# Optimization experiments

Hardware: AMD Instinct MI355X
Metric: run time of the kernel (lower is better)

The kernel has to match this reference:

```python
import jax, jax.numpy as jnp
import numpy as np

NUM_FEATURES = 5
MUL_FACTOR = 2.0


def setup_inputs() -> dict:
    key = jax.random.key(0)
    x = jax.random.normal(key, (4096, 512), dtype=jnp.float32)
    # buffer from __init__: mul_factor ** (arange(F) - F // 2)
    bandwidth_multipliers = (MUL_FACTOR ** (jnp.arange(NUM_FEATURES) - NUM_FEATURES // 2)).astype(jnp.float32)
    return {"x": x, "bandwidth_multipliers": bandwidth_multipliers}


def _cdist(x):
    # pairwise Euclidean distance, p=2
    sq = jnp.sum(x * x, axis=1)
    d2 = sq[:, None] + sq[None, :] - 2.0 * (x @ x.T)
    return jnp.sqrt(jnp.maximum(d2, 0.0))


def reference(x, bandwidth_multipliers):
    d = _cdist(x)  # [N, N]
    n = d.shape[0]
    # heuristic bandwidth on detached distances (self.bandwidth is None)
    bw = jax.lax.stop_gradient(d).sum() / (n * (n - 1))
    bws = bw * bandwidth_multipliers  # [F]
    # exp over F bandwidths, summed: [F, N, N] -> [N, N]
    return jnp.exp(-d[None, :, :] / bws[:, None, None]).sum(axis=0)
```

## Files before the change

### kernel.cpp

```cpp
#include <hip/hip_runtime.h>
#include <cstdint>
#include <cstddef>

#define N_PTS 4096
#define KDIM  512
#define NFEAT 5

typedef __attribute__((ext_vector_type(8))) short bf16x8;
typedef __attribute__((ext_vector_type(4))) float f32x4;
typedef uint32_t u32;

__device__ inline unsigned short f2bf(float f) {
  union { float f; u32 u; } v; v.f = f;
  u32 r = (v.u + 0x7fffu + ((v.u >> 16) & 1u)) >> 16;
  return (unsigned short)r;
}

__device__ inline void bf2f2(u32 u, float& a, float& b) {
  union { u32 u; float f; } x, y;
  x.u = u << 16; y.u = u & 0xffff0000u;
  a = x.f; b = y.f;
}

__device__ inline void load_lds16(const void* g, void* l) {
  __builtin_amdgcn_global_load_lds(
      (const __attribute__((address_space(1))) void*)g,
      (__attribute__((address_space(3))) void*)l, 16, 0, 0);
}

__global__ __launch_bounds__(256) void prep_kernel(const float* __restrict__ X,
                                                   short* __restrict__ Xb,
                                                   float* __restrict__ sq) {
  const int row = blockIdx.x;
  const int t = threadIdx.x;
  const float2 v = ((const float2*)(X + (size_t)row * KDIM))[t];
  short2 b;
  b.x = (short)f2bf(v.x);
  b.y = (short)f2bf(v.y);
  ((short2*)(Xb + (size_t)row * KDIM))[t] = b;
  float s = v.x * v.x + v.y * v.y;
#pragma unroll
  for (int off = 32; off; off >>= 1) s += __shfl_down(s, off);
  __shared__ float ws[4];
  if ((t & 63) == 0) ws[t >> 6] = s;
  __syncthreads();
  if (t == 0) sq[row] = ws[0] + ws[1] + ws[2] + ws[3];
}

__global__ __launch_bounds__(256, 2) void dist_kernel(
    const short* __restrict__ Xb, const float* __restrict__ sq,
    unsigned short* __restrict__ Dw, float* __restrict__ gsum) {
  const int bm = blockIdx.y, bn = blockIdx.x;
  if (bm > bn) return;

  __shared__ short As[128 * 64];
  __shared__ short Bs[128 * 64];
  __shared__ float red[4];

  const int tid = threadIdx.x;
  const int lane = tid & 63;
  const int wid = tid >> 6;
  const int wave_m = wid >> 1, wave_n = wid & 1;
  const int lhi = lane >> 4, llo = lane & 15;

  f32x4 acc[4][4];
#pragma unroll
  for (int i = 0; i < 4; ++i)
#pragma unroll
    for (int j = 0; j < 4; ++j) acc[i][j] = (f32x4){0.f, 0.f, 0.f, 0.f};

  const int srow = tid >> 3;
  const int scol = (tid & 7) * 8;
  const size_t ga0 = (size_t)(bm * 128 + srow) * KDIM + scol;
  const size_t gb0 = (size_t)(bn * 128 + srow) * KDIM + scol;

  for (int kt = 0; kt < KDIM / 64; ++kt) {
    const int koff = kt * 64;
#pragma unroll
    for (int g = 0; g < 4; ++g) {
      load_lds16(Xb + ga0 + (size_t)g * 32 * KDIM + koff, (char*)As + g * 4096 + tid * 16);
      load_lds16(Xb + gb0 + (size_t)g * 32 * KDIM + koff, (char*)Bs + g * 4096 + tid * 16);
    }
    __syncthreads();

    bf16x8 a[2][4], b[2][4];
#pragma unroll
    for (int h = 0; h < 2; ++h)
#pragma unroll
      for (int i = 0; i < 4; ++i) {
        a[h][i] = *(const bf16x8*)&As[(wave_m * 64 + i * 16 + llo) * 64 + h * 32 + lhi * 8];
        b[h][i] = *(const bf16x8*)&Bs[(wave_n * 64 + i * 16 + llo) * 64 + h * 32 + lhi * 8];
      }
#pragma unroll
    for (int h = 0; h < 2; ++h)
#pragma unroll
      for (int i = 0; i < 4; ++i)
#pragma unroll
        for (int j = 0; j < 4; ++j)
          acc[i][j] =
              __builtin_amdgcn_mfma_f32_16x16x32_bf16(a[h][i], b[h][j], acc[i][j], 0, 0, 0);
    __syncthreads();
  }

  float lsum = 0.f;
  const int gi0 = bm * 128 + wave_m * 64;
  const int gj0 = bn * 128 + wave_n * 64;
#pragma unroll
  for (int i = 0; i < 4; ++i) {
#pragma unroll
    for (int r = 0; r < 4; ++r) {
      const int gi = gi0 + i * 16 + lhi * 4 + r;
      const float sqi = sq[gi];
#pragma unroll
      for (int j = 0; j < 4; ++j) {
        const int gj = gj0 + j * 16 + llo;
        float d2 = sqi + sq[gj] - 2.f * acc[i][j][r];
        float dd = sqrtf(fmaxf(d2, 0.f));
        if (gi == gj) dd = 0.f;
        Dw[(size_t)gi * N_PTS + gj] = f2bf(dd);
        lsum += dd;
      }
    }
  }
#pragma unroll
  for (int off = 32; off; off >>= 1) lsum += __shfl_down(lsum, off);
  if (lane == 0) red[wid] = lsum;
  __syncthreads();
  if (tid == 0) {
    const float scale = (bm == bn) ? 1.f : 2.f;
    atomicAdd(gsum, scale * (red[0] + red[1] + red[2] + red[3]));
  }
}

__global__ __launch_bounds__(256) void rbf_kernel(
    const unsigned short* __restrict__ Dw, const float* __restrict__ gsum,
    const float* __restrict__ mult, float* __restrict__ out) {
  const int bm = blockIdx.y, bn = blockIdx.x;
  if (bm > bn) return;

  __shared__ float S[32][132];

  const float bw = *gsum * (1.0f / ((float)N_PTS * (float)(N_PTS - 1)));
  float c[NFEAT];
#pragma unroll
  for (int f = 0; f < NFEAT; ++f) c[f] = -1.0f / (bw * mult[f]);

  const int t = threadIdx.x;
  const int r = t >> 3;
  const int c16 = (t & 7) * 16;
  const int gj0 = bn * 128;
  const int gi_base = bm * 128;

  for (int s = 0; s < 4; ++s) {
    const int gi = gi_base + s * 32 + r;
    const unsigned short* src = Dw + (size_t)gi * N_PTS + gj0 + c16;
    const uint4 p0 = *(const uint4*)src;
    const uint4 p1 = *(const uint4*)(src + 8);

    float v[16];
    bf2f2(p0.x, v[0], v[1]);   bf2f2(p0.y, v[2], v[3]);
    bf2f2(p0.z, v[4], v[5]);   bf2f2(p0.w, v[6], v[7]);
    bf2f2(p1.x, v[8], v[9]);   bf2f2(p1.y, v[10], v[11]);
    bf2f2(p1.z, v[12], v[13]); bf2f2(p1.w, v[14], v[15]);

    float o[16];
#pragma unroll
    for (int e = 0; e < 16; ++e) {
      float a = 0.f;
#pragma unroll
      for (int f = 0; f < NFEAT; ++f) a += __expf(v[e] * c[f]);
      o[e] = a;
    }

    float* drow = out + (size_t)gi * N_PTS + gj0 + c16;
#pragma unroll
    for (int q = 0; q < 4; ++q)
      ((float4*)drow)[q] = (float4){o[q * 4], o[q * 4 + 1], o[q * 4 + 2], o[q * 4 + 3]};

    if (bm != bn) {
#pragma unroll
      for (int q = 0; q < 4; ++q)
        *(float4*)&S[r][c16 + q * 4] =
            (float4){o[q * 4], o[q * 4 + 1], o[q * 4 + 2], o[q * 4 + 3]};
      __syncthreads();
      const int tb = gi_base + s * 32;
      const int k = t & 7;
#pragma unroll
      for (int p = 0; p < 4; ++p) {
        const int cc = p * 32 + (t >> 3);
        float4 q4;
        q4.x = S[k * 4 + 0][cc];
        q4.y = S[k * 4 + 1][cc];
        q4.z = S[k * 4 + 2][cc];
        q4.w = S[k * 4 + 3][cc];
        *(float4*)&out[(size_t)(gj0 + cc) * N_PTS + tb + k * 4] = q4;
      }
      __syncthreads();
    }
  }
}

extern "C" void kernel_launch(void* const* d_in, const int* in_sizes, int n_in,
                              void* d_out, int out_size, void* d_ws, size_t ws_size,
                              hipStream_t stream) {
  const float* X = (const float*)d_in[0];
  const float* mult = (const float*)d_in[1];
  float* out = (float*)d_out;

  char* ws = (char*)d_ws;
  float* gsum = (float*)ws;
  float* sq = (float*)(ws + 1024);
  short* Xb = (short*)(ws + 1024 + N_PTS * sizeof(float));
  unsigned short* Dw = (unsigned short*)(ws + 1024 + N_PTS * sizeof(float) +
                                         (size_t)N_PTS * KDIM * sizeof(short));

  hipMemsetAsync(gsum, 0, 256, stream);
  prep_kernel<<<N_PTS, 256, 0, stream>>>(X, Xb, sq);
  dist_kernel<<<dim3(32, 32), 256, 0, stream>>>(Xb, sq, Dw, gsum);
  rbf_kernel<<<dim3(32, 32), 256, 0, stream>>>(Dw, gsum, mult, out);
}
```

Before: 134.6 us.

## Mirror distance tiles in dist kernel and make RBF pass a flat streaming loop

The distance epilogue now stages each bf16 tile in swizzled LDS (reusing the A/B buffers) and writes both the tile and its transpose to the full distance matrix with coalesced 16-byte stores. This lets the RBF kernel become a simple grid-stride elementwise pass over the whole matrix, with no LDS transpose or scattered stores. The partial sums for the bandwidth now use per-wave atomics instead of a block reduction. The cost is twice as many bf16 distance writes and reads, and four times as many atomics.

Measured after the change: 148.3 us. 1.1x slower.

```diff
diff --git a/kernel.cpp b/kernel.cpp
--- a/kernel.cpp
+++ b/kernel.cpp
@@ -53,9 +53,10 @@
   const int bm = blockIdx.y, bn = blockIdx.x;
   if (bm > bn) return;
 
-  __shared__ short As[128 * 64];
-  __shared__ short Bs[128 * 64];
-  __shared__ float red[4];
+  __shared__ uint4 smem4[2048];
+  short* As = (short*)smem4;
+  short* Bs = (short*)smem4 + 128 * 64;
+  char* T = (char*)smem4;
 
   const int tid = threadIdx.x;
   const int lane = tid & 63;
@@ -103,100 +104,97 @@
   }
 
   float lsum = 0.f;
-  const int gi0 = bm * 128 + wave_m * 64;
-  const int gj0 = bn * 128 + wave_n * 64;
+  const int gi0 = bm * 128, gj0 = bn * 128;
+  const int r_base = wave_m * 64 + lhi * 4;
+  const int c_base = wave_n * 64 + llo;
+  float sqj[4];
+#pragma unroll
+  for (int j = 0; j < 4; ++j) sqj[j] = sq[gj0 + c_base + j * 16];
+
 #pragma unroll
   for (int i = 0; i < 4; ++i) {
 #pragma unroll
-    for (int r = 0; r < 4; ++r) {
-      const int gi = gi0 + i * 16 + lhi * 4 + r;
-      const float sqi = sq[gi];
+    for (int rr = 0; rr < 4; ++rr) {
+      const int r = r_base + i * 16 + rr;
+      const float sqi = sq[gi0 + r];
+      const int swz = (r >> 3) & 15;
+      const int rbyte = r * 256;
 #pragma unroll
       for (int j = 0; j < 4; ++j) {
-        const int gj = gj0 + j * 16 + llo;
-        float d2 = sqi + sq[gj] - 2.f * acc[i][j][r];
+        const int c = c_base + j * 16;
+        float d2 = sqi + sqj[j] - 2.f * acc[i][j][rr];
         float dd = sqrtf(fmaxf(d2, 0.f));
-        if (gi == gj) dd = 0.f;
-        Dw[(size_t)gi * N_PTS + gj] = f2bf(dd);
+        if (gi0 + r == gj0 + c) dd = 0.f;
         lsum += dd;
+        *(unsigned short*)(T + rbyte + (((c >> 3) ^ swz) << 4) + ((c & 7) << 1)) = f2bf(dd);
       }
     }
   }
 #pragma unroll
   for (int off = 32; off; off >>= 1) lsum += __shfl_down(lsum, off);
-  if (lane == 0) red[wid] = lsum;
+  if (lane == 0) {
+    const float scale = (bm == bn) ? 1.f : 2.f;
+    atomicAdd(gsum, scale * lsum);
+  }
   __syncthreads();
-  if (tid == 0) {
-    const float scale = (bm == bn) ? 1.f : 2.f;
-    atomicAdd(gsum, scale * (red[0] + red[1] + red[2] + red[3]));
+
+  const int tA = tid & 15, tB = tid >> 4;
+#pragma unroll
+  for (int s = 0; s < 8; ++s) {
+    const int r = s * 16 + tB;
+    const int g = tA ^ ((r >> 3) & 15);
+    const uint4 v = *(const uint4*)(T + r * 256 + g * 16);
+    *(uint4*)&Dw[(size_t)(gi0 + r) * N_PTS + gj0 + tA * 8] = v;
+  }
+
+  if (bm != bn) {
+#pragma unroll
+    for (int s = 0; s < 8; ++s) {
+      const int mr = s * 16 + tB;
+      const int base = (((mr >> 3) ^ tA) << 4) + ((mr & 7) << 1);
+      u32 p[4];
+#pragma unroll
+      for (int k = 0; k < 4; ++k) {
+        const u32 lo = *(const unsigned short*)(T + (tA * 8 + 2 * k) * 256 + base);
+        const u32 hi = *(const unsigned short*)(T + (tA * 8 + 2 * k + 1) * 256 + base);
+        p[k] = lo | (hi << 16);
+      }
+      *(uint4*)&Dw[(size_t)(gj0 + mr) * N_PTS + gi0 + tA * 8] =
+          (uint4){p[0], p[1], p[2], p[3]};
+    }
   }
 }
 
 __global__ __launch_bounds__(256) void rbf_kernel(
     const unsigned short* __restrict__ Dw, const float* __restrict__ gsum,
     const float* __restrict__ mult, float* __restrict__ out) {
-  const int bm = blockIdx.y, bn = blockIdx.x;
-  if (bm > bn) return;
-
-  __shared__ float S[32][132];
-
   const float bw = *gsum * (1.0f / ((float)N_PTS * (float)(N_PTS - 1)));
   float c[NFEAT];
 #pragma unroll
   for (int f = 0; f < NFEAT; ++f) c[f] = -1.0f / (bw * mult[f]);
 
-  const int t = threadIdx.x;
-  const int r = t >> 3;
-  const int c16 = (t & 7) * 16;
-  const int gj0 = bn * 128;
-  const int gi_base = bm * 128;
-
-  for (int s = 0; s < 4; ++s) {
-    const int gi = gi_base + s * 32 + r;
-    const unsigned short* src = Dw + (size_t)gi * N_PTS + gj0 + c16;
-    const uint4 p0 = *(const uint4*)src;
-    const uint4 p1 = *(const uint4*)(src + 8);
-
-    float v[16];
-    bf2f2(p0.x, v[0], v[1]);   bf2f2(p0.y, v[2], v[3]);
-    bf2f2(p0.z, v[4], v[5]);   bf2f2(p0.w, v[6], v[7]);
-    bf2f2(p1.x, v[8], v[9]);   bf2f2(p1.y, v[10], v[11]);
-    bf2f2(p1.z, v[12], v[13]); bf2f2(p1.w, v[14], v[15]);
-
-    float o[16];
-#pragma unroll
-    for (int e = 0; e < 16; ++e) {
+  const size_t total = (size_t)N_PTS * N_PTS / 8;
+  const size_t stride = (size_t)gridDim.x * blockDim.x;
+  const uint4* D8 = (const uint4*)Dw;
+  for (size_t idx = (size_t)blockIdx.x * blockDim.x + threadIdx.x; idx < total;
+       idx += stride) {
+    const uint4 pck = D8[idx];
+    float v[8];
+    bf2f2(pck.x, v[0], v[1]);
+    bf2f2(pck.y, v[2], v[3]);
+    bf2f2(pck.z, v[4], v[5]);
+    bf2f2(pck.w, v[6], v[7]);
+    float o[8];
+#pragma unroll
+    for (int e = 0; e < 8; ++e) {
       float a = 0.f;
 #pragma unroll
       for (int f = 0; f < NFEAT; ++f) a += __expf(v[e] * c[f]);
       o[e] = a;
     }
-
-    float* drow = out + (size_t)gi * N_PTS + gj0 + c16;
-#pragma unroll
-    for (int q = 0; q < 4; ++q)
-      ((float4*)drow)[q] = (float4){o[q * 4], o[q * 4 + 1], o[q * 4 + 2], o[q * 4 + 3]};
-
-    if (bm != bn) {
-#pragma unroll
-      for (int q = 0; q < 4; ++q)
-        *(float4*)&S[r][c16 + q * 4] =
-            (float4){o[q * 4], o[q * 4 + 1], o[q * 4 + 2], o[q * 4 + 3]};
-      __syncthreads();
-      const int tb = gi_base + s * 32;
-      const int k = t & 7;
-#pragma unroll
-      for (int p = 0; p < 4; ++p) {
-        const int cc = p * 32 + (t >> 3);
-        float4 q4;
-        q4.x = S[k * 4 + 0][cc];
-        q4.y = S[k * 4 + 1][cc];
-        q4.z = S[k * 4 + 2][cc];
-        q4.w = S[k * 4 + 3][cc];
-        *(float4*)&out[(size_t)(gj0 + cc) * N_PTS + tb + k * 4] = q4;
-      }
-      __syncthreads();
-    }
+    float4* dst = (float4*)(out + idx * 8);
+    dst[0] = (float4){o[0], o[1], o[2], o[3]};
+    dst[1] = (float4){o[4], o[5], o[6], o[7]};
   }
 }
 
@@ -217,5 +215,5 @@
   hipMemsetAsync(gsum, 0, 256, stream);
   prep_kernel<<<N_PTS, 256, 0, stream>>>(X, Xb, sq);
   dist_kernel<<<dim3(32, 32), 256, 0, stream>>>(Xb, sq, Dw, gsum);
-  rbf_kernel<<<dim3(32, 32), 256, 0, stream>>>(Dw, gsum, mult, out);
-}
+  rbf_kernel<<<2048, 256, 0, stream>>>(Dw, gsum, mult, out);
+}
```
